# Kernel optimization log

Hardware: AMD Instinct MI355X
Metric: run time of the kernel (lower is better)

## Reference

```python
import jax
import jax.numpy as jnp
import numpy as np

N = 1024   # n_neurons (input size == hidden size)
L = 2      # n_layers of the stacked nn.RNN
T = 8      # n_tsteps (number of chained RNN+Linear blocks)
B = 1024   # x.shape[0]; acts as the RNN sequence length (batch=1 inside nn.RNN)


def setup_inputs() -> dict:
    key = jax.random.key(0)
    ks = jax.random.split(key, 7)
    s = 1.0 / np.sqrt(N)  # torch default init bound for RNN/Linear with fan_in=N
    x = jax.random.normal(ks[0], (B, T, N), dtype=jnp.float32)
    rnn_Wih = jax.random.uniform(ks[1], (T, L, N, N), minval=-s, maxval=s, dtype=jnp.float32)
    rnn_Whh = jax.random.uniform(ks[2], (T, L, N, N), minval=-s, maxval=s, dtype=jnp.float32)
    rnn_bih = jax.random.uniform(ks[3], (T, L, N), minval=-s, maxval=s, dtype=jnp.float32)
    rnn_bhh = jax.random.uniform(ks[4], (T, L, N), minval=-s, maxval=s, dtype=jnp.float32)
    lin_W = jax.random.uniform(ks[5], (T, N, N), minval=-s, maxval=s, dtype=jnp.float32)
    lin_b = jax.random.uniform(ks[6], (T, N), minval=-s, maxval=s, dtype=jnp.float32)
    return {"x": x, "rnn_Wih": rnn_Wih, "rnn_Whh": rnn_Whh,
            "rnn_bih": rnn_bih, "rnn_bhh": rnn_bhh,
            "lin_W": lin_W, "lin_b": lin_b}


def _rnn_layer(seq, Wih, Whh, bih, bhh):
    """Single tanh-RNN layer over sequence `seq` [S, N] with batch=1, h0=0."""
    def step(h, xt):
        h_new = jnp.tanh(xt @ Wih.T + bih + h @ Whh.T + bhh)
        return h_new, h_new
    _, out = jax.lax.scan(step, jnp.zeros((Wih.shape[0],), seq.dtype), seq)
    return out  # [S, N]


def reference(x, rnn_Wih, rnn_Whh, rnn_bih, rnn_bhh, lin_W, lin_b):
    # x: [B, T, N]. Torch code feeds x[:, 0, :] (shape [B, 1, N]) into nn.RNN
    # (batch_first=False), so B is the sequence length and batch size is 1.
    n_tsteps, n_layers = rnn_Wih.shape[0], rnn_Wih.shape[1]
    seq = x[:, 0, :]  # [B, N]
    outs = []
    for t in range(n_tsteps):
        for l in range(n_layers):
            seq = _rnn_layer(seq, rnn_Wih[t, l], rnn_Whh[t, l],
                             rnn_bih[t, l], rnn_bhh[t, l])
        seq = seq @ lin_W[t].T + lin_b[t]  # nn.Linear
        outs.append(seq)
    return jnp.stack(outs, axis=1)  # [B, T, N]
```

## Files before the change

kernel.cpp:

```cpp
#include <hip/hip_runtime.h>
#include <hip/hip_fp16.h>

#define NN 1024
#define NST 16
#define WPS 16
#define WROWS 64

typedef _Float16 v2h __attribute__((ext_vector_type(2)));
typedef unsigned int uint;
typedef unsigned long long u64;
typedef unsigned int u32x4 __attribute__((ext_vector_type(4)));

__device__ __half g_W[NST][NN][2048];
__device__ float g_bias[NST][NN];
__device__ u64 g_S[NST][NN][512];
__device__ float g_Hout[8][NN * NN];

__device__ __forceinline__ v2h as_v2h(uint u) {
  union { uint u; v2h h; } c; c.u = u; return c.h;
}
__device__ __forceinline__ uint pk2(float a, float b) {
  union { v2h h; uint u; } c; c.h.x = (_Float16)a; c.h.y = (_Float16)b; return c.u;
}
__device__ __forceinline__ int swzu(int u) {
  return (u & ~7) | ((u + (u >> 3)) & 7);
}
__device__ __forceinline__ u32x4 ld_opaque16(const __half* p) {
  u32x4 r;
  asm volatile("global_load_dwordx4 %0, %1, off" : "=v"(r) : "v"(p));
  return r;
}
__device__ __forceinline__ float fdot4(u32x4 w, u32x4 v, float a) {
  a = __builtin_amdgcn_fdot2(as_v2h(w.x), as_v2h(v.x), a, false);
  a = __builtin_amdgcn_fdot2(as_v2h(w.y), as_v2h(v.y), a, false);
  a = __builtin_amdgcn_fdot2(as_v2h(w.z), as_v2h(v.z), a, false);
  a = __builtin_amdgcn_fdot2(as_v2h(w.w), as_v2h(v.w), a, false);
  return a;
}
__device__ __forceinline__ float dpp_reduce16(float v) {
  int t;
  t = __builtin_amdgcn_update_dpp(0, __float_as_int(v), 0x111, 0xF, 0xF, true); v += __int_as_float(t);
  t = __builtin_amdgcn_update_dpp(0, __float_as_int(v), 0x112, 0xF, 0xF, true); v += __int_as_float(t);
  t = __builtin_amdgcn_update_dpp(0, __float_as_int(v), 0x114, 0xF, 0xF, true); v += __int_as_float(t);
  t = __builtin_amdgcn_update_dpp(0, __float_as_int(v), 0x118, 0xF, 0xF, true); v += __int_as_float(t);
  return v;
}

__global__ void k_init() {
  const size_t n = (size_t)NST * NN * 512;
  size_t i = (size_t)blockIdx.x * blockDim.x + threadIdx.x;
  const size_t stride = (size_t)gridDim.x * blockDim.x;
  u64* p = &g_S[0][0][0];
  for (; i < n; i += stride) p[i] = 0ull;
}

__global__ void k_pack(const float* __restrict__ Wih, const float* __restrict__ Whh) {
  const size_t total = (size_t)NST * NN * NN;
  size_t i = (size_t)blockIdx.x * blockDim.x + threadIdx.x;
  const size_t stride = (size_t)gridDim.x * blockDim.x;
  for (; i < total; i += stride) {
    const int st = (int)(i >> 20);
    const int m = (int)(i >> 10) & 1023;
    const int k = (int)i & 1023;
    g_W[st][m][1024 + k] = __float2half(Whh[i]);
    const int t = st >> 1, l = st & 1;
    if (l == 1 || t == 0) g_W[st][m][k] = __float2half(Wih[i]);
  }
}

__global__ __launch_bounds__(256) void k_fold(const float* __restrict__ Wih,
                                              const float* __restrict__ linW) {
  const int tm1 = blockIdx.z;
  const int st = (tm1 + 1) * 2;
  const float* A = Wih + (size_t)st * NN * NN;
  const float* B = linW + (size_t)tm1 * NN * NN;
  __shared__ float sA[16][68];
  __shared__ float sB[16][68];
  const int tid = threadIdx.x;
  const int tx = tid & 15, ty = tid >> 4;
  const int bm = blockIdx.y << 6, bn = blockIdx.x << 6;
  const int lm = tid & 63, lk = (tid >> 6) << 2;
  const int rr = tid >> 4, c4 = (tid & 15) << 2;
  float acc[4][4] = {};
  for (int k0 = 0; k0 < NN; k0 += 16) {
    const float4 av = *(const float4*)&A[(size_t)(bm + lm) * NN + k0 + lk];
    const float4 bv = *(const float4*)&B[(size_t)(k0 + rr) * NN + bn + c4];
    __syncthreads();
    sA[lk + 0][lm] = av.x; sA[lk + 1][lm] = av.y; sA[lk + 2][lm] = av.z; sA[lk + 3][lm] = av.w;
    sB[rr][c4 + 0] = bv.x; sB[rr][c4 + 1] = bv.y; sB[rr][c4 + 2] = bv.z; sB[rr][c4 + 3] = bv.w;
    __syncthreads();
    #pragma unroll
    for (int kk = 0; kk < 16; ++kk) {
      const float4 a4 = *(const float4*)&sA[kk][ty << 2];
      const float4 b4 = *(const float4*)&sB[kk][tx << 2];
      const float aa[4] = {a4.x, a4.y, a4.z, a4.w};
      const float bb[4] = {b4.x, b4.y, b4.z, b4.w};
      #pragma unroll
      for (int i = 0; i < 4; ++i)
        #pragma unroll
        for (int j = 0; j < 4; ++j) acc[i][j] += aa[i] * bb[j];
    }
  }
  #pragma unroll
  for (int i = 0; i < 4; ++i)
    #pragma unroll
    for (int j = 0; j < 4; ++j)
      g_W[st][bm + (ty << 2) + i][bn + (tx << 2) + j] = __float2half(acc[i][j]);
}

__global__ __launch_bounds__(256) void k_bias(const float* __restrict__ Wih,
    const float* __restrict__ bih, const float* __restrict__ bhh,
    const float* __restrict__ linb) {
  const int st = blockIdx.x, t = st >> 1, l = st & 1;
  const int tid = threadIdx.x;
  __shared__ float slb[NN];
  const bool folded = (l == 0 && t > 0);
  if (folded)
    for (int k = tid; k < NN; k += 256) slb[k] = linb[(size_t)(t - 1) * NN + k];
  __syncthreads();
  for (int m = tid; m < NN; m += 256) {
    float b = bih[(size_t)st * NN + m] + bhh[(size_t)st * NN + m];
    if (folded) {
      const float* wr = Wih + (size_t)st * NN * NN + (size_t)m * NN;
      float s0 = 0, s1 = 0, s2 = 0, s3 = 0;
      for (int k = 0; k < NN; k += 4) {
        const float4 w = *(const float4*)&wr[k];
        s0 += w.x * slb[k]; s1 += w.y * slb[k + 1];
        s2 += w.z * slb[k + 2]; s3 += w.w * slb[k + 3];
      }
      b += (s0 + s1) + (s2 + s3);
    }
    g_bias[st][m] = b;
  }
}

__global__ __launch_bounds__(512)
__attribute__((amdgpu_waves_per_eu(2, 2)))
void k_phase(const float* __restrict__ x) {
  __shared__ __align__(16) unsigned char comb[2][4096];
  const int tid = threadIdx.x;
  const int bid = blockIdx.x;
  const int st = ((bid & 7) << 1) + (bid >> 7);
  const int wg = (bid >> 3) & 15;
  const int woff = wg << 6;
  const int i = tid >> 4;
  const int c = tid & 15;

#define LDX(RR, JJ) ld_opaque16(&g_W[st][woff + 2 * i + (RR)][64 * c + 8 * (JJ)])
#define LDH(RR, JJ) ld_opaque16(&g_W[st][woff + 2 * i + (RR)][1024 + 64 * c + 8 * (JJ)])
  u32x4 x00 = LDX(0,0), x01 = LDX(0,1), x02 = LDX(0,2), x03 = LDX(0,3);
  u32x4 x04 = LDX(0,4), x05 = LDX(0,5), x06 = LDX(0,6), x07 = LDX(0,7);
  u32x4 x10 = LDX(1,0), x11 = LDX(1,1), x12 = LDX(1,2), x13 = LDX(1,3);
  u32x4 x14 = LDX(1,4), x15 = LDX(1,5), x16 = LDX(1,6), x17 = LDX(1,7);
  u32x4 h00 = LDH(0,0), h01 = LDH(0,1), h02 = LDH(0,2), h03 = LDH(0,3);
  u32x4 h04 = LDH(0,4), h05 = LDH(0,5), h06 = LDH(0,6), h07 = LDH(0,7);
  u32x4 h10 = LDH(1,0), h11 = LDH(1,1), h12 = LDH(1,2), h13 = LDH(1,3);
  u32x4 h14 = LDH(1,4), h15 = LDH(1,5), h16 = LDH(1,6), h17 = LDH(1,7);
#undef LDX
#undef LDH
  asm volatile("s_waitcnt vmcnt(0)" ::: "memory");
  __builtin_amdgcn_sched_barrier(0);

  const float2 breg = *(const float2*)&g_bias[st][woff + 2 * i];

  const int uW = tid >> 2, off4 = (tid & 3) << 2;
  const int wbx = swzu(uW) * 16 + off4;
  const int wbh = swzu(128 + uW) * 16 + off4;
  const int slot_pub = (woff >> 1) + i;

  for (int s = 0; s < NN; ++s) {
    unsigned char* cb = comb[s & 1];
    uint xu = 0;
    if (st == 0) {
      const float2 xv = *(const float2*)&x[(size_t)s * 8192 + 2 * tid];
      xu = pk2(xv.x, xv.y);
    } else {
      const u64* pu = &g_S[st - 1][s][tid];
      for (;;) {
        const u64 a = __hip_atomic_load(pu, __ATOMIC_RELAXED, __HIP_MEMORY_SCOPE_AGENT);
        if (a >> 32) { xu = (uint)a; break; }
        __builtin_amdgcn_s_sleep(1);
      }
    }
    *(uint*)&cb[wbx] = xu;
    __syncthreads();

    float p0 = 0.f, p1 = 0.f;
#define XSTEP(JJ, Q0, Q1) { \
      const u32x4 v = *(const u32x4*)&cb[swzu(8 * c + (JJ)) * 16]; \
      p0 = fdot4(Q0, v, p0); p1 = fdot4(Q1, v, p1); }
    XSTEP(0, x00, x10) XSTEP(1, x01, x11) XSTEP(2, x02, x12) XSTEP(3, x03, x13)
    XSTEP(4, x04, x14) XSTEP(5, x05, x15) XSTEP(6, x06, x16) XSTEP(7, x07, x17)
#undef XSTEP

    uint hu = 0;
    if (s > 0) {
      const u64* po = &g_S[st][s - 1][tid];
      for (;;) {
        const u64 b = __hip_atomic_load(po, __ATOMIC_RELAXED, __HIP_MEMORY_SCOPE_AGENT);
        if (b >> 32) { hu = (uint)b; break; }
      }
    }
    *(uint*)&cb[wbh] = hu;
    __syncthreads();

#define HSTEP(JJ, Q0, Q1) { \
      const u32x4 v = *(const u32x4*)&cb[swzu(128 + 8 * c + (JJ)) * 16]; \
      p0 = fdot4(Q0, v, p0); p1 = fdot4(Q1, v, p1); }
    HSTEP(0, h00, h10) HSTEP(1, h01, h11) HSTEP(2, h02, h12) HSTEP(3, h03, h13)
    HSTEP(4, h04, h14) HSTEP(5, h05, h15) HSTEP(6, h06, h16) HSTEP(7, h07, h17)
#undef HSTEP

    p0 = dpp_reduce16(p0);
    p1 = dpp_reduce16(p1);
    if (c == 15) {
      const float hv0 = tanhf(p0 + breg.x);
      const float hv1 = tanhf(p1 + breg.y);
      const u64 pv = (1ull << 32) | (u64)pk2(hv0, hv1);
      __hip_atomic_store(&g_S[st][s][slot_pub], pv,
                         __ATOMIC_RELAXED, __HIP_MEMORY_SCOPE_AGENT);
      if (st & 1)
        *(float2*)&g_Hout[st >> 1][(size_t)s * NN + woff + 2 * i] =
            make_float2(hv0, hv1);
    }
  }
}

__global__ __launch_bounds__(256) void k_out(const float* __restrict__ linW,
    const float* __restrict__ linb, float* __restrict__ out) {
  const int t = blockIdx.z;
  const float* A = g_Hout[t];
  const float* B = linW + (size_t)t * NN * NN;
  __shared__ float sA[16][68];
  __shared__ float sB[16][68];
  const int tid = threadIdx.x;
  const int tx = tid & 15, ty = tid >> 4;
  const int bm = blockIdx.y << 6, bn = blockIdx.x << 6;
  const int lm = tid & 63, lk = (tid >> 6) << 2;
  float acc[4][4] = {};
  for (int k0 = 0; k0 < NN; k0 += 16) {
    const float4 av = *(const float4*)&A[(size_t)(bm + lm) * NN + k0 + lk];
    const float4 bv = *(const float4*)&B[(size_t)(bn + lm) * NN + k0 + lk];
    __syncthreads();
    sA[lk + 0][lm] = av.x; sA[lk + 1][lm] = av.y; sA[lk + 2][lm] = av.z; sA[lk + 3][lm] = av.w;
    sB[lk + 0][lm] = bv.x; sB[lk + 1][lm] = bv.y; sB[lk + 2][lm] = bv.z; sB[lk + 3][lm] = bv.w;
    __syncthreads();
    #pragma unroll
    for (int kk = 0; kk < 16; ++kk) {
      const float4 a4 = *(const float4*)&sA[kk][ty << 2];
      const float4 b4 = *(const float4*)&sB[kk][tx << 2];
      const float aa[4] = {a4.x, a4.y, a4.z, a4.w};
      const float bb[4] = {b4.x, b4.y, b4.z, b4.w};
      #pragma unroll
      for (int i = 0; i < 4; ++i)
        #pragma unroll
        for (int j = 0; j < 4; ++j) acc[i][j] += aa[i] * bb[j];
    }
  }
  const int n0 = bn + (tx << 2);
  float bias[4];
  #pragma unroll
  for (int j = 0; j < 4; ++j) bias[j] = linb[(size_t)t * NN + n0 + j];
  #pragma unroll
  for (int i = 0; i < 4; ++i) {
    const int m = bm + (ty << 2) + i;
    float4 o;
    o.x = acc[i][0] + bias[0]; o.y = acc[i][1] + bias[1];
    o.z = acc[i][2] + bias[2]; o.w = acc[i][3] + bias[3];
    *(float4*)&out[(size_t)m * 8192 + (size_t)t * NN + n0] = o;
  }
}

extern "C" void kernel_launch(void* const* d_in, const int* in_sizes, int n_in,
                              void* d_out, int out_size, void* d_ws, size_t ws_size,
                              hipStream_t stream) {
  (void)in_sizes; (void)n_in; (void)out_size; (void)d_ws; (void)ws_size;
  const float* x    = (const float*)d_in[0];
  const float* Wih  = (const float*)d_in[1];
  const float* Whh  = (const float*)d_in[2];
  const float* bih  = (const float*)d_in[3];
  const float* bhh  = (const float*)d_in[4];
  const float* linW = (const float*)d_in[5];
  const float* linb = (const float*)d_in[6];
  float* out = (float*)d_out;

  k_init<<<2048, 256, 0, stream>>>();
  k_pack<<<2048, 256, 0, stream>>>(Wih, Whh);
  k_fold<<<dim3(16, 16, 7), 256, 0, stream>>>(Wih, linW);
  k_bias<<<16, 256, 0, stream>>>(Wih, bih, bhh, linb);
  k_phase<<<256, 512, 0, stream>>>(x);
  k_out<<<dim3(16, 16, 8), 256, 0, stream>>>(linW, linb, out);
}
```

Baseline: 2.374 ms.

## Move fold and output GEMMs to fp16 MFMA and parallelize bias kernel

The weight-fold GEMM (Wih·linW) and the final output Linear GEMM move from FP32 SIMT tiles to fp16 MFMA 16x16x32 with 128x128 tiles. To feed them, k_pack now also writes fp16 copies of the layer-0 Wih and linW, and k_out converts hidden states to fp16 while loading them. k_bias is spread over a 2D grid so each thread handles one row instead of looping. These GEMMs are small next to the sequential k_phase recurrence, and the fp16 output GEMM lowers precision.

```diff
diff --git a/kernel.cpp b/kernel.cpp
--- a/kernel.cpp
+++ b/kernel.cpp
@@ -3,10 +3,10 @@
 
 #define NN 1024
 #define NST 16
-#define WPS 16
-#define WROWS 64
 
 typedef _Float16 v2h __attribute__((ext_vector_type(2)));
+typedef _Float16 f16x8 __attribute__((ext_vector_type(8)));
+typedef float f32x4 __attribute__((ext_vector_type(4)));
 typedef unsigned int uint;
 typedef unsigned long long u64;
 typedef unsigned int u32x4 __attribute__((ext_vector_type(4)));
@@ -15,6 +15,8 @@
 __device__ float g_bias[NST][NN];
 __device__ u64 g_S[NST][NN][512];
 __device__ float g_Hout[8][NN * NN];
+__device__ _Float16 g_Wih16F[7][NN * NN];
+__device__ _Float16 g_linW16[8][NN * NN];
 
 __device__ __forceinline__ v2h as_v2h(uint u) {
   union { uint u; v2h h; } c; c.u = u; return c.h;
@@ -54,58 +56,144 @@
   for (; i < n; i += stride) p[i] = 0ull;
 }
 
-__global__ void k_pack(const float* __restrict__ Wih, const float* __restrict__ Whh) {
+__global__ void k_pack(const float* __restrict__ Wih, const float* __restrict__ Whh,
+                       const float* __restrict__ linW) {
   const size_t total = (size_t)NST * NN * NN;
-  size_t i = (size_t)blockIdx.x * blockDim.x + threadIdx.x;
   const size_t stride = (size_t)gridDim.x * blockDim.x;
-  for (; i < total; i += stride) {
+  for (size_t i = (size_t)blockIdx.x * blockDim.x + threadIdx.x; i < total; i += stride) {
     const int st = (int)(i >> 20);
     const int m = (int)(i >> 10) & 1023;
     const int k = (int)i & 1023;
     g_W[st][m][1024 + k] = __float2half(Whh[i]);
     const int t = st >> 1, l = st & 1;
     if (l == 1 || t == 0) g_W[st][m][k] = __float2half(Wih[i]);
-  }
-}
-
-__global__ __launch_bounds__(256) void k_fold(const float* __restrict__ Wih,
-                                              const float* __restrict__ linW) {
+    else g_Wih16F[t - 1][(size_t)m * NN + k] = (_Float16)Wih[i];
+  }
+  const size_t ltotal = (size_t)8 * NN * NN;
+  _Float16* lw = &g_linW16[0][0];
+  for (size_t i = (size_t)blockIdx.x * blockDim.x + threadIdx.x; i < ltotal; i += stride)
+    lw[i] = (_Float16)linW[i];
+}
+
+#define GPAD 40
+
+__global__ __launch_bounds__(256) void k_fold(int dummy) {
   const int tm1 = blockIdx.z;
   const int st = (tm1 + 1) * 2;
-  const float* A = Wih + (size_t)st * NN * NN;
-  const float* B = linW + (size_t)tm1 * NN * NN;
-  __shared__ float sA[16][68];
-  __shared__ float sB[16][68];
+  const _Float16* A = &g_Wih16F[tm1][0];
+  const _Float16* B = &g_linW16[tm1][0];
+  __shared__ _Float16 sA[128 * GPAD];
+  __shared__ _Float16 sB[128 * GPAD];
   const int tid = threadIdx.x;
-  const int tx = tid & 15, ty = tid >> 4;
-  const int bm = blockIdx.y << 6, bn = blockIdx.x << 6;
-  const int lm = tid & 63, lk = (tid >> 6) << 2;
-  const int rr = tid >> 4, c4 = (tid & 15) << 2;
-  float acc[4][4] = {};
-  for (int k0 = 0; k0 < NN; k0 += 16) {
-    const float4 av = *(const float4*)&A[(size_t)(bm + lm) * NN + k0 + lk];
-    const float4 bv = *(const float4*)&B[(size_t)(k0 + rr) * NN + bn + c4];
-    __syncthreads();
-    sA[lk + 0][lm] = av.x; sA[lk + 1][lm] = av.y; sA[lk + 2][lm] = av.z; sA[lk + 3][lm] = av.w;
-    sB[rr][c4 + 0] = bv.x; sB[rr][c4 + 1] = bv.y; sB[rr][c4 + 2] = bv.z; sB[rr][c4 + 3] = bv.w;
-    __syncthreads();
-    #pragma unroll
-    for (int kk = 0; kk < 16; ++kk) {
-      const float4 a4 = *(const float4*)&sA[kk][ty << 2];
-      const float4 b4 = *(const float4*)&sB[kk][tx << 2];
-      const float aa[4] = {a4.x, a4.y, a4.z, a4.w};
-      const float bb[4] = {b4.x, b4.y, b4.z, b4.w};
-      #pragma unroll
-      for (int i = 0; i < 4; ++i)
-        #pragma unroll
-        for (int j = 0; j < 4; ++j) acc[i][j] += aa[i] * bb[j];
-    }
-  }
+  const int bm = blockIdx.y << 7, bn = blockIdx.x << 7;
+  const int lane = tid & 63, wid = tid >> 6;
+  const int wm = wid >> 1, wn = wid & 1;
+  const int lr = lane & 15, kc = (lane >> 4) << 3;
+  f32x4 acc[4][4] = {};
+  const int arow = tid >> 1, ahalf = tid & 1;
+  const int bj = tid >> 3, bcs = tid & 7;
+
+  for (int k0 = 0; k0 < NN; k0 += 32) {
+    __syncthreads();
+    {
+      const u32x4 a0 = *(const u32x4*)&A[(size_t)(bm + arow) * NN + k0 + 16 * ahalf];
+      const u32x4 a1 = *(const u32x4*)&A[(size_t)(bm + arow) * NN + k0 + 16 * ahalf + 8];
+      u32x4* dst = (u32x4*)&sA[arow * GPAD + 16 * ahalf];
+      dst[0] = a0; dst[1] = a1;
+      union { u32x4 v; _Float16 h[8]; } ua, ub;
+      ua.v = *(const u32x4*)&B[(size_t)(k0 + bj) * NN + bn + 16 * bcs];
+      ub.v = *(const u32x4*)&B[(size_t)(k0 + bj) * NN + bn + 16 * bcs + 8];
+      #pragma unroll
+      for (int q = 0; q < 8; ++q) sB[(16 * bcs + q) * GPAD + bj] = ua.h[q];
+      #pragma unroll
+      for (int q = 0; q < 8; ++q) sB[(16 * bcs + 8 + q) * GPAD + bj] = ub.h[q];
+    }
+    __syncthreads();
+    f16x8 af[4], bf[4];
+    #pragma unroll
+    for (int f = 0; f < 4; ++f) {
+      af[f] = *(const f16x8*)&sA[(wm * 64 + f * 16 + lr) * GPAD + kc];
+      bf[f] = *(const f16x8*)&sB[(wn * 64 + f * 16 + lr) * GPAD + kc];
+    }
+    #pragma unroll
+    for (int fm = 0; fm < 4; ++fm)
+      #pragma unroll
+      for (int fn = 0; fn < 4; ++fn)
+        acc[fm][fn] = __builtin_amdgcn_mfma_f32_16x16x32_f16(af[fm], bf[fn], acc[fm][fn], 0, 0, 0);
+  }
+  const int orow = (lane >> 4) << 2, ocol = lane & 15;
   #pragma unroll
-  for (int i = 0; i < 4; ++i)
-    #pragma unroll
-    for (int j = 0; j < 4; ++j)
-      g_W[st][bm + (ty << 2) + i][bn + (tx << 2) + j] = __float2half(acc[i][j]);
+  for (int fm = 0; fm < 4; ++fm)
+    #pragma unroll
+    for (int fn = 0; fn < 4; ++fn) {
+      const int gr = bm + wm * 64 + fm * 16 + orow;
+      const int gc = bn + wn * 64 + fn * 16 + ocol;
+      #pragma unroll
+      for (int r = 0; r < 4; ++r)
+        g_W[st][gr + r][gc] = __float2half(acc[fm][fn][r]);
+    }
+}
+
+__global__ __launch_bounds__(256) void k_out(const float* __restrict__ linb,
+                                             float* __restrict__ out) {
+  const int t = blockIdx.z;
+  const float* A = &g_Hout[t][0];
+  const _Float16* B = &g_linW16[t][0];
+  __shared__ _Float16 sA[128 * GPAD];
+  __shared__ _Float16 sB[128 * GPAD];
+  const int tid = threadIdx.x;
+  const int bm = blockIdx.y << 7, bn = blockIdx.x << 7;
+  const int lane = tid & 63, wid = tid >> 6;
+  const int wm = wid >> 1, wn = wid & 1;
+  const int lr = lane & 15, kc = (lane >> 4) << 3;
+  f32x4 acc[4][4] = {};
+  const int arow = tid >> 1, ahalf = tid & 1;
+
+  for (int k0 = 0; k0 < NN; k0 += 32) {
+    __syncthreads();
+    {
+      const float* srcA = &A[(size_t)(bm + arow) * NN + k0 + 16 * ahalf];
+      const float4 f0 = *(const float4*)&srcA[0];
+      const float4 f1 = *(const float4*)&srcA[4];
+      const float4 f2 = *(const float4*)&srcA[8];
+      const float4 f3 = *(const float4*)&srcA[12];
+      u32x4 o0, o1;
+      o0.x = pk2(f0.x, f0.y); o0.y = pk2(f0.z, f0.w);
+      o0.z = pk2(f1.x, f1.y); o0.w = pk2(f1.z, f1.w);
+      o1.x = pk2(f2.x, f2.y); o1.y = pk2(f2.z, f2.w);
+      o1.z = pk2(f3.x, f3.y); o1.w = pk2(f3.z, f3.w);
+      u32x4* dstA = (u32x4*)&sA[arow * GPAD + 16 * ahalf];
+      dstA[0] = o0; dstA[1] = o1;
+      const u32x4 b0 = *(const u32x4*)&B[(size_t)(bn + arow) * NN + k0 + 16 * ahalf];
+      const u32x4 b1 = *(const u32x4*)&B[(size_t)(bn + arow) * NN + k0 + 16 * ahalf + 8];
+      u32x4* dstB = (u32x4*)&sB[arow * GPAD + 16 * ahalf];
+      dstB[0] = b0; dstB[1] = b1;
+    }
+    __syncthreads();
+    f16x8 af[4], bf[4];
+    #pragma unroll
+    for (int f = 0; f < 4; ++f) {
+      af[f] = *(const f16x8*)&sA[(wm * 64 + f * 16 + lr) * GPAD + kc];
+      bf[f] = *(const f16x8*)&sB[(wn * 64 + f * 16 + lr) * GPAD + kc];
+    }
+    #pragma unroll
+    for (int fm = 0; fm < 4; ++fm)
+      #pragma unroll
+      for (int fn = 0; fn < 4; ++fn)
+        acc[fm][fn] = __builtin_amdgcn_mfma_f32_16x16x32_f16(af[fm], bf[fn], acc[fm][fn], 0, 0, 0);
+  }
+  const int orow = (lane >> 4) << 2, ocol = lane & 15;
+  #pragma unroll
+  for (int fm = 0; fm < 4; ++fm)
+    #pragma unroll
+    for (int fn = 0; fn < 4; ++fn) {
+      const int gr = bm + wm * 64 + fm * 16 + orow;
+      const int gc = bn + wn * 64 + fn * 16 + ocol;
+      const float lb = linb[(size_t)t * NN + gc];
+      #pragma unroll
+      for (int r = 0; r < 4; ++r)
+        out[(size_t)(gr + r) * 8192 + (size_t)t * NN + gc] = acc[fm][fn][r] + lb;
+    }
 }
 
 __global__ __launch_bounds__(256) void k_bias(const float* __restrict__ Wih,
@@ -113,25 +201,24 @@
     const float* __restrict__ linb) {
   const int st = blockIdx.x, t = st >> 1, l = st & 1;
   const int tid = threadIdx.x;
+  const int m = (blockIdx.y << 8) + tid;
   __shared__ float slb[NN];
   const bool folded = (l == 0 && t > 0);
   if (folded)
     for (int k = tid; k < NN; k += 256) slb[k] = linb[(size_t)(t - 1) * NN + k];
   __syncthreads();
-  for (int m = tid; m < NN; m += 256) {
-    float b = bih[(size_t)st * NN + m] + bhh[(size_t)st * NN + m];
-    if (folded) {
-      const float* wr = Wih + (size_t)st * NN * NN + (size_t)m * NN;
-      float s0 = 0, s1 = 0, s2 = 0, s3 = 0;
-      for (int k = 0; k < NN; k += 4) {
-        const float4 w = *(const float4*)&wr[k];
-        s0 += w.x * slb[k]; s1 += w.y * slb[k + 1];
-        s2 += w.z * slb[k + 2]; s3 += w.w * slb[k + 3];
-      }
-      b += (s0 + s1) + (s2 + s3);
-    }
-    g_bias[st][m] = b;
-  }
+  float b = bih[(size_t)st * NN + m] + bhh[(size_t)st * NN + m];
+  if (folded) {
+    const float* wr = Wih + (size_t)st * NN * NN + (size_t)m * NN;
+    float s0 = 0, s1 = 0, s2 = 0, s3 = 0;
+    for (int k = 0; k < NN; k += 4) {
+      const float4 w = *(const float4*)&wr[k];
+      s0 += w.x * slb[k]; s1 += w.y * slb[k + 1];
+      s2 += w.z * slb[k + 2]; s3 += w.w * slb[k + 3];
+    }
+    b += (s0 + s1) + (s2 + s3);
+  }
+  g_bias[st][m] = b;
 }
 
 __global__ __launch_bounds__(512)
@@ -226,51 +313,6 @@
   }
 }
 
-__global__ __launch_bounds__(256) void k_out(const float* __restrict__ linW,
-    const float* __restrict__ linb, float* __restrict__ out) {
-  const int t = blockIdx.z;
-  const float* A = g_Hout[t];
-  const float* B = linW + (size_t)t * NN * NN;
-  __shared__ float sA[16][68];
-  __shared__ float sB[16][68];
-  const int tid = threadIdx.x;
-  const int tx = tid & 15, ty = tid >> 4;
-  const int bm = blockIdx.y << 6, bn = blockIdx.x << 6;
-  const int lm = tid & 63, lk = (tid >> 6) << 2;
-  float acc[4][4] = {};
-  for (int k0 = 0; k0 < NN; k0 += 16) {
-    const float4 av = *(const float4*)&A[(size_t)(bm + lm) * NN + k0 + lk];
-    const float4 bv = *(const float4*)&B[(size_t)(bn + lm) * NN + k0 + lk];
-    __syncthreads();
-    sA[lk + 0][lm] = av.x; sA[lk + 1][lm] = av.y; sA[lk + 2][lm] = av.z; sA[lk + 3][lm] = av.w;
-    sB[lk + 0][lm] = bv.x; sB[lk + 1][lm] = bv.y; sB[lk + 2][lm] = bv.z; sB[lk + 3][lm] = bv.w;
-    __syncthreads();
-    #pragma unroll
-    for (int kk = 0; kk < 16; ++kk) {
-      const float4 a4 = *(const float4*)&sA[kk][ty << 2];
-      const float4 b4 = *(const float4*)&sB[kk][tx << 2];
-      const float aa[4] = {a4.x, a4.y, a4.z, a4.w};
-      const float bb[4] = {b4.x, b4.y, b4.z, b4.w};
-      #pragma unroll
-      for (int i = 0; i < 4; ++i)
-        #pragma unroll
-        for (int j = 0; j < 4; ++j) acc[i][j] += aa[i] * bb[j];
-    }
-  }
-  const int n0 = bn + (tx << 2);
-  float bias[4];
-  #pragma unroll
-  for (int j = 0; j < 4; ++j) bias[j] = linb[(size_t)t * NN + n0 + j];
-  #pragma unroll
-  for (int i = 0; i < 4; ++i) {
-    const int m = bm + (ty << 2) + i;
-    float4 o;
-    o.x = acc[i][0] + bias[0]; o.y = acc[i][1] + bias[1];
-    o.z = acc[i][2] + bias[2]; o.w = acc[i][3] + bias[3];
-    *(float4*)&out[(size_t)m * 8192 + (size_t)t * NN + n0] = o;
-  }
-}
-
 extern "C" void kernel_launch(void* const* d_in, const int* in_sizes, int n_in,
                               void* d_out, int out_size, void* d_ws, size_t ws_size,
                               hipStream_t stream) {
@@ -285,9 +327,9 @@
   float* out = (float*)d_out;
 
   k_init<<<2048, 256, 0, stream>>>();
-  k_pack<<<2048, 256, 0, stream>>>(Wih, Whh);
-  k_fold<<<dim3(16, 16, 7), 256, 0, stream>>>(Wih, linW);
-  k_bias<<<16, 256, 0, stream>>>(Wih, bih, bhh, linb);
+  k_pack<<<2048, 256, 0, stream>>>(Wih, Whh, linW);
+  k_fold<<<dim3(8, 8, 7), 256, 0, stream>>>(0);
+  k_bias<<<dim3(16, 4), 256, 0, stream>>>(Wih, bih, bhh, linb);
   k_phase<<<256, 512, 0, stream>>>(x);
-  k_out<<<dim3(16, 16, 8), 256, 0, stream>>>(linW, linb, out);
-}
+  k_out<<<dim3(8, 8, 8), 256, 0, stream>>>(linb, out);
+}
```

Result: faster. 1.969 ms (-17.0%).
